# Kernel optimization log

Measured on AMD Instinct MI355X. Metric: run time of the kernel, lower is better.

The kernel has to match this reference:

```python
import jax, jax.numpy as jnp
from jax import lax
import numpy as np

D_MODEL = 1024
N_HEADS = 16
D_STATE = D_MODEL // N_HEADS  # 64
EPS = 1e-6


def setup_inputs() -> dict:
    key = jax.random.key(0)
    ks = jax.random.split(key, 8)
    B, S = 4, 4096
    s = 1.0 / np.sqrt(D_MODEL)
    return {
        "x": jax.random.normal(ks[0], (B, S, D_MODEL), dtype=jnp.float32),
        "state": jnp.zeros((B, N_HEADS, D_STATE), dtype=jnp.float32),
        "norm_w": jnp.ones((D_MODEL,), dtype=jnp.float32),
        "Wp": jax.random.normal(ks[1], (D_MODEL, 3 * N_HEADS * D_STATE), dtype=jnp.float32) * s,
        "bp": jax.random.normal(ks[2], (3 * N_HEADS * D_STATE,), dtype=jnp.float32) * 0.01,
        "Wg": jax.random.normal(ks[3], (D_MODEL, D_MODEL), dtype=jnp.float32) * s,
        "bg": jax.random.normal(ks[4], (D_MODEL,), dtype=jnp.float32) * 0.01,
        "Wo": jax.random.normal(ks[5], (D_MODEL, D_MODEL), dtype=jnp.float32) * s,
        "bo": jax.random.normal(ks[6], (D_MODEL,), dtype=jnp.float32) * 0.01,
    }


def reference(x, state, norm_w, Wp, bp, Wg, bg, Wo, bo):
    B, S, D = x.shape
    # RMSNorm
    rms = jnp.sqrt(jnp.mean(x * x, axis=-1, keepdims=True) + EPS)
    xn = norm_w * x / rms
    # input-dependent gate and SSM parameters (all per-timestep, vectorized)
    gate = jax.nn.sigmoid(xn @ Wg + bg)                        # (B,S,D)
    p = (xn @ Wp + bp).reshape(B, S, N_HEADS, 3, D_STATE)
    delta = jax.nn.sigmoid(p[..., 0, :])                       # (B,S,H,Ds)
    Bt = p[..., 1, :]
    Ct = p[..., 2, :]
    # sequential recurrence h_{t+1} = delta_t * h_t + B_t via lax.scan over time
    def step(h, db):
        d, b = db
        h = d * h + b
        return h, h
    dT = jnp.moveaxis(delta, 1, 0)  # (S,B,H,Ds)
    bT = jnp.moveaxis(Bt, 1, 0)
    new_state, hs = lax.scan(step, state, (dT, bT))
    hs = jnp.moveaxis(hs, 0, 1)     # (B,S,H,Ds)
    ssm = (Ct * hs).reshape(B, S, D)
    mixed = gate * ssm + (1.0 - gate) * xn
    y = mixed @ Wo + bo + x         # out_proj + residual (dropout=0)
    return y, new_state
```

## Files before the change

### kernel.cpp

```cpp
#include <hip/hip_runtime.h>
#include <hip/hip_bf16.h>
#include <cstdint>
#include <cstddef>

#define D_MODEL 1024
#define N_HEADS 16
#define D_STATE 64
#define SEQ 4096
#define BATCH 4
#define M_TOK (BATCH * SEQ)
#define N1 4096
#define CLEN 64
#define NCH (SEQ / CLEN)
#define NCHAN (BATCH * D_MODEL)

typedef __attribute__((ext_vector_type(8))) short bf16x8;
typedef __attribute__((ext_vector_type(4))) short bf16x4;
typedef __attribute__((ext_vector_type(4))) float f32x4;

__device__ __forceinline__ float sigmoidf_(float x) {
    return 1.0f / (1.0f + __expf(-x));
}
__device__ __forceinline__ float b2f(short s) {
    union { float f; unsigned u; } v; v.u = ((unsigned)(unsigned short)s) << 16;
    return v.f;
}
__device__ __forceinline__ short f2b(float f) {
    __hip_bfloat16 h = __float2bfloat16(f);
    return *(short*)&h;
}

__device__ __forceinline__ void async_load16(const void* g, void* l) {
    __builtin_amdgcn_global_load_lds(
        (__attribute__((address_space(1))) void*)(g),
        (__attribute__((address_space(3))) void*)(l), 16, 0, 0);
}

__global__ __launch_bounds__(256) void prep_kernel(
    const float* __restrict__ Wg, const float* __restrict__ Wp,
    const float* __restrict__ Wo,
    const float* __restrict__ x, const float* __restrict__ norm_w,
    __hip_bfloat16* __restrict__ W1T, __hip_bfloat16* __restrict__ WoT,
    __hip_bfloat16* __restrict__ xn)
{
    __shared__ float tile[32][33];
    __shared__ float red[4];
    const int bid = blockIdx.x;
    const int tid = threadIdx.x;

    if (bid < 5120) {
        const float* src; __hip_bfloat16* dst; int N, bx, by, perm;
        if (bid < 1024)      { src = Wg; dst = W1T; N = 1024; bx = bid & 31;          by = bid >> 5;          perm = 0; }
        else if (bid < 4096) { int l = bid - 1024; src = Wp; dst = W1T; N = 3072; bx = l % 96; by = l / 96;   perm = 1; }
        else                 { int l = bid - 4096; src = Wo; dst = WoT; N = 1024; bx = l & 31; by = l >> 5;   perm = 0; }
        int n0 = bx * 32, k0 = by * 32;
        int tx = tid & 31, ty = tid >> 5;
#pragma unroll
        for (int j = 0; j < 32; j += 8)
            tile[ty + j][tx] = src[(size_t)(k0 + ty + j) * N + n0 + tx];
        __syncthreads();
#pragma unroll
        for (int j = 0; j < 32; j += 8) {
            int n = n0 + ty + j;
            int row;
            if (perm) {
                int ht = n >> 6;
                row = 1024 + (ht % 3) * 1024 + (ht / 3) * 64 + (n & 63);
            } else row = n;
            dst[(size_t)row * D_MODEL + k0 + tx] = __float2bfloat16(tile[tx][ty + j]);
        }
    } else {
        int m = bid - 5120;
        const float4* xr = (const float4*)(x + (size_t)m * D_MODEL);
        float4 v = xr[tid];
        float ss = v.x * v.x + v.y * v.y + v.z * v.z + v.w * v.w;
#pragma unroll
        for (int o = 32; o >= 1; o >>= 1) ss += __shfl_xor(ss, o, 64);
        int wave = tid >> 6, lane = tid & 63;
        if (lane == 0) red[wave] = ss;
        __syncthreads();
        float tot = red[0] + red[1] + red[2] + red[3];
        float scale = rsqrtf(tot * (1.0f / D_MODEL) + 1e-6f);
        const float4* wr = (const float4*)norm_w;
        float4 wv = wr[tid];
        __hip_bfloat16 o4[4];
        o4[0] = __float2bfloat16(wv.x * v.x * scale);
        o4[1] = __float2bfloat16(wv.y * v.y * scale);
        o4[2] = __float2bfloat16(wv.z * v.z * scale);
        o4[3] = __float2bfloat16(wv.w * v.w * scale);
        *(uint64_t*)(xn + (size_t)m * D_MODEL + tid * 4) = *(uint64_t*)o4;
    }
}

template <int MODE>
__global__ __launch_bounds__(512, 2) void gemm256(
    const __hip_bfloat16* __restrict__ A,
    const __hip_bfloat16* __restrict__ Bt,
    const float* __restrict__ bias0,
    const float* __restrict__ bias1,
    void* __restrict__ outp, int N, int K)
{
    extern __shared__ short lds[];
    const int tid = threadIdx.x;
    const int wave = tid >> 6, lane = tid & 63;
    const int fr = lane & 15, fq = lane >> 4;
    const int frx = fr & 7;
    const int wm = (wave >> 2) * 128;
    const int wn = (wave & 3) * 64;

    const int gx = gridDim.x;
    const int nwg = gx * gridDim.y;
    const int orig = blockIdx.y * gx + blockIdx.x;
    const int swz = (orig & 7) * (nwg >> 3) + (orig >> 3);
    const int m0 = (swz / gx) * 256;
    const int n0 = (swz % gx) * 256;

    const int rb = tid >> 3, p8 = tid & 7;
    const int lsl = p8 ^ (rb & 7);
    const short* Ag0 = (const short*)A + (size_t)(m0 + rb) * K + lsl * 8;
    const short* Bg0 = (const short*)Bt + (size_t)(n0 + rb) * K + lsl * 8;
    const int stL = rb * 64 + p8 * 8;

    const int laneA = (wm + fr) * 128;
    const int laneB = (wn + fr) * 128;
    const int F0 = (fq ^ frx) * 16;
    const int F1 = ((4 + fq) ^ frx) * 16;

    const int NT = K >> 6;

    f32x4 acc[2][4][4];
#pragma unroll
    for (int h = 0; h < 2; ++h)
#pragma unroll
        for (int i = 0; i < 4; ++i)
#pragma unroll
            for (int j = 0; j < 4; ++j)
                acc[h][i][j] = (f32x4){0.f, 0.f, 0.f, 0.f};

    {
        short* la = lds;
        short* lb = lds + 16384;
        async_load16(Bg0 + (size_t)(0 * 64) * K, lb + stL + 0 * 4096);
        async_load16(Bg0 + (size_t)(1 * 64) * K, lb + stL + 1 * 4096);
        async_load16(Bg0 + (size_t)(2 * 64) * K, lb + stL + 2 * 4096);
        async_load16(Bg0 + (size_t)(3 * 64) * K, lb + stL + 3 * 4096);
        async_load16(Ag0 + (size_t)(0 * 64) * K, la + stL + 0 * 4096);
        async_load16(Ag0 + (size_t)(2 * 64) * K, la + stL + 2 * 4096);
        async_load16(Ag0 + (size_t)(1 * 64) * K, la + stL + 1 * 4096);
        async_load16(Ag0 + (size_t)(3 * 64) * K, la + stL + 3 * 4096);
    }
    asm volatile("s_waitcnt vmcnt(2)" ::: "memory");
    __builtin_amdgcn_s_barrier();
    __builtin_amdgcn_sched_barrier(0);

#define RD(base, off) (*(const bf16x8*)((base) + (off)))
#define STAGE_A(c) async_load16(AgN + (size_t)((c) * 64) * K, laN + stL + (c) * 4096)
#define STAGE_B(c) async_load16(BgN + (size_t)((c) * 64) * K, lbN + stL + (c) * 4096)

    bf16x8 afA[4][2], afB[4][2], b0[2][2], b1[2][2];

    {
        const char* bA0 = (const char*)lds + laneA + F0;
        const char* bA1 = (const char*)lds + laneA + F1;
        const char* bB0 = (const char*)(lds + 16384) + laneB + F0;
        const char* bB1 = (const char*)(lds + 16384) + laneB + F1;
#pragma unroll
        for (int i = 0; i < 4; ++i) { afA[i][0] = RD(bA0, i * 2048); afA[i][1] = RD(bA1, i * 2048); }
#pragma unroll
        for (int j = 0; j < 2; ++j) { b0[j][0] = RD(bB0, j * 2048); b0[j][1] = RD(bB1, j * 2048); }
    }

    for (int t = 0; t < NT; ++t) {
        const short* Ab = lds + ((t & 1) ? 32768 : 0);
        const short* Bb = Ab + 16384;
        short* laN = lds + ((t & 1) ? 0 : 32768);
        short* lbN = laN + 16384;
        const short* AgN = Ag0 + (size_t)(t + 1) * 64;
        const short* BgN = Bg0 + (size_t)(t + 1) * 64;
        const bool pf = (t + 1 < NT);
        const char* bA0 = (const char*)Ab + laneA + F0;
        const char* bA1 = (const char*)Ab + laneA + F1;
        const char* bB0 = (const char*)Bb + laneB + F0;
        const char* bB1 = (const char*)Bb + laneB + F1;

        if (pf) { STAGE_B(0); STAGE_B(1); }
#pragma unroll
        for (int j = 0; j < 2; ++j) { b1[j][0] = RD(bB0, (2 + j) * 2048); b1[j][1] = RD(bB1, (2 + j) * 2048); }
        __builtin_amdgcn_s_setprio(1);
#pragma unroll
        for (int i = 0; i < 4; ++i)
#pragma unroll
            for (int j = 0; j < 2; ++j) {
                acc[0][i][j] = __builtin_amdgcn_mfma_f32_16x16x32_bf16(afA[i][0], b0[j][0], acc[0][i][j], 0, 0, 0);
                acc[0][i][j] = __builtin_amdgcn_mfma_f32_16x16x32_bf16(afA[i][1], b0[j][1], acc[0][i][j], 0, 0, 0);
            }
        __builtin_amdgcn_s_setprio(0);
        __builtin_amdgcn_sched_barrier(0);

        if (pf) { STAGE_B(2); STAGE_B(3); }
        if (pf) { asm volatile("s_waitcnt vmcnt(4)" ::: "memory"); }
        else    { asm volatile("s_waitcnt vmcnt(0)" ::: "memory"); }
        __builtin_amdgcn_s_barrier();
        __builtin_amdgcn_sched_barrier(0);
#pragma unroll
        for (int i = 0; i < 4; ++i) { afB[i][0] = RD(bA0, 8192 + i * 2048); afB[i][1] = RD(bA1, 8192 + i * 2048); }
        __builtin_amdgcn_s_setprio(1);
#pragma unroll
        for (int i = 0; i < 4; ++i)
#pragma unroll
            for (int j = 0; j < 2; ++j) {
                acc[0][i][2 + j] = __builtin_amdgcn_mfma_f32_16x16x32_bf16(afA[i][0], b1[j][0], acc[0][i][2 + j], 0, 0, 0);
                acc[0][i][2 + j] = __builtin_amdgcn_mfma_f32_16x16x32_bf16(afA[i][1], b1[j][1], acc[0][i][2 + j], 0, 0, 0);
            }
        __builtin_amdgcn_s_setprio(0);
        __builtin_amdgcn_sched_barrier(0);

        if (pf) { STAGE_A(0); STAGE_A(2); }
        __builtin_amdgcn_s_setprio(1);
#pragma unroll
        for (int i = 0; i < 4; ++i)
#pragma unroll
            for (int j = 0; j < 2; ++j) {
                acc[1][i][j] = __builtin_amdgcn_mfma_f32_16x16x32_bf16(afB[i][0], b0[j][0], acc[1][i][j], 0, 0, 0);
                acc[1][i][j] = __builtin_amdgcn_mfma_f32_16x16x32_bf16(afB[i][1], b0[j][1], acc[1][i][j], 0, 0, 0);
            }
        __builtin_amdgcn_s_setprio(0);
        __builtin_amdgcn_sched_barrier(0);

        if (pf) {
            STAGE_A(1); STAGE_A(3);
            asm volatile("s_waitcnt vmcnt(2)" ::: "memory");
            __builtin_amdgcn_s_barrier();
            __builtin_amdgcn_sched_barrier(0);
            const char* nA0 = (const char*)laN + laneA + F0;
            const char* nA1 = (const char*)laN + laneA + F1;
            const char* nB0 = (const char*)lbN + laneB + F0;
            const char* nB1 = (const char*)lbN + laneB + F1;
#pragma unroll
            for (int i = 0; i < 4; ++i) { afA[i][0] = RD(nA0, i * 2048); afA[i][1] = RD(nA1, i * 2048); }
#pragma unroll
            for (int j = 0; j < 2; ++j) { b0[j][0] = RD(nB0, j * 2048); b0[j][1] = RD(nB1, j * 2048); }
        }
        __builtin_amdgcn_s_setprio(1);
#pragma unroll
        for (int i = 0; i < 4; ++i)
#pragma unroll
            for (int j = 0; j < 2; ++j) {
                acc[1][i][2 + j] = __builtin_amdgcn_mfma_f32_16x16x32_bf16(afB[i][0], b1[j][0], acc[1][i][2 + j], 0, 0, 0);
                acc[1][i][2 + j] = __builtin_amdgcn_mfma_f32_16x16x32_bf16(afB[i][1], b1[j][1], acc[1][i][2 + j], 0, 0, 0);
            }
        __builtin_amdgcn_s_setprio(0);
        __builtin_amdgcn_sched_barrier(0);
    }
#undef RD
#undef STAGE_A
#undef STAGE_B

    if constexpr (MODE == 0) {
        __hip_bfloat16* O = (__hip_bfloat16*)outp;
        float bv[4];
#pragma unroll
        for (int j = 0; j < 4; ++j) {
            int gcol = n0 + wn + j * 16 + fr;
            if (gcol < D_MODEL) bv[j] = bias0[gcol];
            else {
                int q = gcol - D_MODEL;
                int tt = q >> 10, hd = q & 1023;
                bv[j] = bias1[(hd >> 6) * 192 + tt * 64 + (hd & 63)];
            }
        }
#pragma unroll
        for (int h = 0; h < 2; ++h)
#pragma unroll
            for (int i = 0; i < 4; ++i)
#pragma unroll
                for (int r = 0; r < 4; ++r) {
                    int grow = m0 + wm + h * 64 + i * 16 + fq * 4 + r;
                    __hip_bfloat16* orow = O + (size_t)grow * N + n0 + wn + fr;
#pragma unroll
                    for (int j = 0; j < 4; ++j)
                        orow[j * 16] = __float2bfloat16(acc[h][i][j][r] + bv[j]);
                }
    } else {
        float* O = (float*)outp;
#pragma unroll
        for (int h = 0; h < 2; ++h)
#pragma unroll
            for (int i = 0; i < 4; ++i)
#pragma unroll
                for (int r = 0; r < 4; ++r) {
                    int grow = m0 + wm + h * 64 + i * 16 + fq * 4 + r;
#pragma unroll
                    for (int j = 0; j < 4; ++j) {
                        int gcol = n0 + wn + j * 16 + fr;
                        O[(size_t)grow * N + gcol] =
                            acc[h][i][j][r] + bias0[gcol] + bias1[(size_t)grow * D_MODEL + gcol];
                    }
                }
    }
}

__global__ __launch_bounds__(256) void scan_part1(
    const __hip_bfloat16* __restrict__ out1,
    float* __restrict__ Abuf, float* __restrict__ Bbuf)
{
    int g = blockIdx.x * 256 + threadIdx.x;
    int cg = g & 1023;
    int c = g >> 10;
    int chan0 = cg * 4;
    int b = chan0 >> 10, hd0 = chan0 & 1023;
    size_t tok0 = (size_t)b * SEQ + (size_t)c * CLEN;
    const short* pd = (const short*)out1 + tok0 * N1 + D_MODEL + hd0;
    float a[4] = {1.f, 1.f, 1.f, 1.f};
    float hl[4] = {0.f, 0.f, 0.f, 0.f};
#pragma unroll 4
    for (int s = 0; s < CLEN; s++) {
        bf16x4 dv = *(const bf16x4*)pd;
        bf16x4 bv = *(const bf16x4*)(pd + 1024);
#pragma unroll
        for (int k = 0; k < 4; k++) {
            float sd = sigmoidf_(b2f(dv[k]));
            a[k] *= sd;
            hl[k] = sd * hl[k] + b2f(bv[k]);
        }
        pd += N1;
    }
    *(f32x4*)&Abuf[c * NCHAN + chan0] = (f32x4){a[0], a[1], a[2], a[3]};
    *(f32x4*)&Bbuf[c * NCHAN + chan0] = (f32x4){hl[0], hl[1], hl[2], hl[3]};
}

__global__ __launch_bounds__(256) void scan_apply(
    const __hip_bfloat16* __restrict__ out1,
    const __hip_bfloat16* __restrict__ xn,
    const float* __restrict__ Abuf, const float* __restrict__ Bbuf,
    const float* __restrict__ state,
    __hip_bfloat16* __restrict__ mixed, float* __restrict__ new_state)
{
    int g = blockIdx.x * 256 + threadIdx.x;
    int cg = g & 1023;
    int c = g >> 10;
    int chan0 = cg * 4;
    int b = chan0 >> 10, hd0 = chan0 & 1023;
    size_t tok0 = (size_t)b * SEQ + (size_t)c * CLEN;

    f32x4 hp4 = *(const f32x4*)&state[chan0];
    for (int cc = 0; cc < c; ++cc) {
        f32x4 av = *(const f32x4*)&Abuf[cc * NCHAN + chan0];
        f32x4 bv = *(const f32x4*)&Bbuf[cc * NCHAN + chan0];
        hp4 = av * hp4 + bv;
    }
    float hp[4] = {hp4[0], hp4[1], hp4[2], hp4[3]};

    const short* rbase = (const short*)out1 + tok0 * N1;
    const short* xb = (const short*)xn + tok0 * D_MODEL + hd0;
    short* mb = (short*)mixed + tok0 * D_MODEL + hd0;
#pragma unroll 4
    for (int s = 0; s < CLEN; s++) {
        bf16x4 dv = *(const bf16x4*)(rbase + D_MODEL + hd0);
        bf16x4 bv = *(const bf16x4*)(rbase + 2048 + hd0);
        bf16x4 cv = *(const bf16x4*)(rbase + 3072 + hd0);
        bf16x4 gv = *(const bf16x4*)(rbase + hd0);
        bf16x4 xv = *(const bf16x4*)xb;
        bf16x4 ov;
#pragma unroll
        for (int k = 0; k < 4; k++) {
            float sd = sigmoidf_(b2f(dv[k]));
            hp[k] = sd * hp[k] + b2f(bv[k]);
            float gg = sigmoidf_(b2f(gv[k]));
            ov[k] = f2b(gg * (b2f(cv[k]) * hp[k]) + (1.0f - gg) * b2f(xv[k]));
        }
        *(bf16x4*)mb = ov;
        rbase += N1;
        xb += D_MODEL;
        mb += D_MODEL;
    }
    if (c == NCH - 1)
        *(f32x4*)&new_state[chan0] = (f32x4){hp[0], hp[1], hp[2], hp[3]};
}

extern "C" void kernel_launch(void* const* d_in, const int* in_sizes, int n_in,
                              void* d_out, int out_size, void* d_ws, size_t ws_size,
                              hipStream_t stream) {
    const float* x      = (const float*)d_in[0];
    const float* state  = (const float*)d_in[1];
    const float* norm_w = (const float*)d_in[2];
    const float* Wp     = (const float*)d_in[3];
    const float* bp     = (const float*)d_in[4];
    const float* Wg     = (const float*)d_in[5];
    const float* bg     = (const float*)d_in[6];
    const float* Wo     = (const float*)d_in[7];
    const float* bo     = (const float*)d_in[8];
    float* out = (float*)d_out;

    __hip_bfloat16* W1T   = (__hip_bfloat16*)d_ws;
    __hip_bfloat16* WoT   = W1T + (size_t)N1 * D_MODEL;
    __hip_bfloat16* xnb   = WoT + (size_t)D_MODEL * D_MODEL;
    __hip_bfloat16* out1  = xnb + (size_t)M_TOK * D_MODEL;
    __hip_bfloat16* mixed = out1 + (size_t)M_TOK * N1;
    float* Abuf = (float*)(mixed + (size_t)M_TOK * D_MODEL);
    float* Bbuf = Abuf + (size_t)NCHAN * NCH;

    static bool attr_set = false;
    if (!attr_set) {
        hipFuncSetAttribute(reinterpret_cast<const void*>(&gemm256<0>),
                            hipFuncAttributeMaxDynamicSharedMemorySize, 131072);
        hipFuncSetAttribute(reinterpret_cast<const void*>(&gemm256<1>),
                            hipFuncAttributeMaxDynamicSharedMemorySize, 131072);
        attr_set = true;
    }

    prep_kernel<<<5120 + M_TOK, 256, 0, stream>>>(
        Wg, Wp, Wo, x, norm_w, W1T, WoT, xnb);

    gemm256<0><<<dim3(N1 / 256, M_TOK / 256), 512, 131072, stream>>>(
        xnb, W1T, bg, bp, (void*)out1, N1, D_MODEL);

    scan_part1<<<(NCHAN / 4 * NCH) / 256, 256, 0, stream>>>(out1, Abuf, Bbuf);

    scan_apply<<<(NCHAN / 4 * NCH) / 256, 256, 0, stream>>>(
        out1, xnb, Abuf, Bbuf, state, mixed, out + (size_t)M_TOK * D_MODEL);

    gemm256<1><<<dim3(D_MODEL / 256, M_TOK / 256), 512, 131072, stream>>>(
        mixed, WoT, bo, x, (void*)out, D_MODEL, D_MODEL);
}
```

Baseline: 392.7 us.

## Restage GEMM loads two tiles ahead, shrink scan chunks, write mixed in place

The GEMM prefetch is restructured so whole 64-wide K tiles are loaded two iterations ahead into the alternate LDS buffer, with a single barrier per iteration instead of interleaved partial stages. The scan chunk length is halved to expose more parallelism in the chunked recurrence, and the mixed output now overwrites the normalized-input buffer in place, dropping a separate workspace. The RMSNorm part of the prep kernel now processes one row per wave, removing the shared-memory reduction and block sync. The deeper prefetch trades finer-grained overlap for fewer barriers, and shorter chunks add more serial carry work per chunk in the apply pass.

```diff
diff --git a/kernel.cpp b/kernel.cpp
--- a/kernel.cpp
+++ b/kernel.cpp
@@ -10,7 +10,7 @@
 #define BATCH 4
 #define M_TOK (BATCH * SEQ)
 #define N1 4096
-#define CLEN 64
+#define CLEN 32
 #define NCH (SEQ / CLEN)
 #define NCHAN (BATCH * D_MODEL)
 
@@ -44,15 +44,14 @@
     __hip_bfloat16* __restrict__ xn)
 {
     __shared__ float tile[32][33];
-    __shared__ float red[4];
     const int bid = blockIdx.x;
     const int tid = threadIdx.x;
 
     if (bid < 5120) {
         const float* src; __hip_bfloat16* dst; int N, bx, by, perm;
-        if (bid < 1024)      { src = Wg; dst = W1T; N = 1024; bx = bid & 31;          by = bid >> 5;          perm = 0; }
-        else if (bid < 4096) { int l = bid - 1024; src = Wp; dst = W1T; N = 3072; bx = l % 96; by = l / 96;   perm = 1; }
-        else                 { int l = bid - 4096; src = Wo; dst = WoT; N = 1024; bx = l & 31; by = l >> 5;   perm = 0; }
+        if (bid < 1024)      { src = Wg; dst = W1T; N = 1024; bx = bid & 31;        by = bid >> 5;        perm = 0; }
+        else if (bid < 4096) { int l = bid - 1024; src = Wp; dst = W1T; N = 3072; bx = l % 96; by = l / 96; perm = 1; }
+        else                 { int l = bid - 4096; src = Wo; dst = WoT; N = 1024; bx = l & 31; by = l >> 5; perm = 0; }
         int n0 = bx * 32, k0 = by * 32;
         int tx = tid & 31, ty = tid >> 5;
 #pragma unroll
@@ -70,25 +69,30 @@
             dst[(size_t)row * D_MODEL + k0 + tx] = __float2bfloat16(tile[tx][ty + j]);
         }
     } else {
-        int m = bid - 5120;
+        int m = (bid - 5120) * 4 + (tid >> 6);
+        int lane = tid & 63;
         const float4* xr = (const float4*)(x + (size_t)m * D_MODEL);
-        float4 v = xr[tid];
-        float ss = v.x * v.x + v.y * v.y + v.z * v.z + v.w * v.w;
+        float4 v[4];
+        float ss = 0.f;
+#pragma unroll
+        for (int q = 0; q < 4; ++q) {
+            v[q] = xr[lane + 64 * q];
+            ss += v[q].x * v[q].x + v[q].y * v[q].y + v[q].z * v[q].z + v[q].w * v[q].w;
+        }
 #pragma unroll
         for (int o = 32; o >= 1; o >>= 1) ss += __shfl_xor(ss, o, 64);
-        int wave = tid >> 6, lane = tid & 63;
-        if (lane == 0) red[wave] = ss;
-        __syncthreads();
-        float tot = red[0] + red[1] + red[2] + red[3];
-        float scale = rsqrtf(tot * (1.0f / D_MODEL) + 1e-6f);
+        float scale = rsqrtf(ss * (1.0f / D_MODEL) + 1e-6f);
         const float4* wr = (const float4*)norm_w;
-        float4 wv = wr[tid];
-        __hip_bfloat16 o4[4];
-        o4[0] = __float2bfloat16(wv.x * v.x * scale);
-        o4[1] = __float2bfloat16(wv.y * v.y * scale);
-        o4[2] = __float2bfloat16(wv.z * v.z * scale);
-        o4[3] = __float2bfloat16(wv.w * v.w * scale);
-        *(uint64_t*)(xn + (size_t)m * D_MODEL + tid * 4) = *(uint64_t*)o4;
+#pragma unroll
+        for (int q = 0; q < 4; ++q) {
+            float4 wv = wr[lane + 64 * q];
+            __hip_bfloat16 o4[4];
+            o4[0] = __float2bfloat16(wv.x * v[q].x * scale);
+            o4[1] = __float2bfloat16(wv.y * v[q].y * scale);
+            o4[2] = __float2bfloat16(wv.z * v[q].z * scale);
+            o4[3] = __float2bfloat16(wv.w * v[q].w * scale);
+            *(uint64_t*)(xn + (size_t)m * D_MODEL + (lane + 64 * q) * 4) = *(uint64_t*)o4;
+        }
     }
 }
 
@@ -137,28 +141,30 @@
             for (int j = 0; j < 4; ++j)
                 acc[h][i][j] = (f32x4){0.f, 0.f, 0.f, 0.f};
 
-    {
-        short* la = lds;
-        short* lb = lds + 16384;
-        async_load16(Bg0 + (size_t)(0 * 64) * K, lb + stL + 0 * 4096);
-        async_load16(Bg0 + (size_t)(1 * 64) * K, lb + stL + 1 * 4096);
-        async_load16(Bg0 + (size_t)(2 * 64) * K, lb + stL + 2 * 4096);
-        async_load16(Bg0 + (size_t)(3 * 64) * K, lb + stL + 3 * 4096);
-        async_load16(Ag0 + (size_t)(0 * 64) * K, la + stL + 0 * 4096);
-        async_load16(Ag0 + (size_t)(2 * 64) * K, la + stL + 2 * 4096);
-        async_load16(Ag0 + (size_t)(1 * 64) * K, la + stL + 1 * 4096);
-        async_load16(Ag0 + (size_t)(3 * 64) * K, la + stL + 3 * 4096);
-    }
-    asm volatile("s_waitcnt vmcnt(2)" ::: "memory");
+#define STAGE8(Tt, base)                                                   \
+    {                                                                      \
+        short* la_ = (base);                                               \
+        short* lb_ = (base) + 16384;                                       \
+        const short* Ag_ = Ag0 + (size_t)(Tt) * 64;                        \
+        const short* Bg_ = Bg0 + (size_t)(Tt) * 64;                        \
+        async_load16(Bg_ + (size_t)(0 * 64) * K, lb_ + stL + 0 * 4096);    \
+        async_load16(Bg_ + (size_t)(1 * 64) * K, lb_ + stL + 1 * 4096);    \
+        async_load16(Bg_ + (size_t)(2 * 64) * K, lb_ + stL + 2 * 4096);    \
+        async_load16(Bg_ + (size_t)(3 * 64) * K, lb_ + stL + 3 * 4096);    \
+        async_load16(Ag_ + (size_t)(0 * 64) * K, la_ + stL + 0 * 4096);    \
+        async_load16(Ag_ + (size_t)(1 * 64) * K, la_ + stL + 1 * 4096);    \
+        async_load16(Ag_ + (size_t)(2 * 64) * K, la_ + stL + 2 * 4096);    \
+        async_load16(Ag_ + (size_t)(3 * 64) * K, la_ + stL + 3 * 4096);    \
+    }
+#define RD(base, off) (*(const bf16x8*)((base) + (off)))
+
+    STAGE8(0, lds);
+    STAGE8(1, lds + 32768);
+    asm volatile("s_waitcnt vmcnt(8)" ::: "memory");
     __builtin_amdgcn_s_barrier();
     __builtin_amdgcn_sched_barrier(0);
 
-#define RD(base, off) (*(const bf16x8*)((base) + (off)))
-#define STAGE_A(c) async_load16(AgN + (size_t)((c) * 64) * K, laN + stL + (c) * 4096)
-#define STAGE_B(c) async_load16(BgN + (size_t)((c) * 64) * K, lbN + stL + (c) * 4096)
-
     bf16x8 afA[4][2], afB[4][2], b0[2][2], b1[2][2];
-
     {
         const char* bA0 = (const char*)lds + laneA + F0;
         const char* bA1 = (const char*)lds + laneA + F1;
@@ -171,19 +177,16 @@
     }
 
     for (int t = 0; t < NT; ++t) {
-        const short* Ab = lds + ((t & 1) ? 32768 : 0);
+        const int par = t & 1;
+        const short* Ab = lds + (par ? 32768 : 0);
         const short* Bb = Ab + 16384;
-        short* laN = lds + ((t & 1) ? 0 : 32768);
-        short* lbN = laN + 16384;
-        const short* AgN = Ag0 + (size_t)(t + 1) * 64;
-        const short* BgN = Bg0 + (size_t)(t + 1) * 64;
-        const bool pf = (t + 1 < NT);
         const char* bA0 = (const char*)Ab + laneA + F0;
         const char* bA1 = (const char*)Ab + laneA + F1;
         const char* bB0 = (const char*)Bb + laneB + F0;
         const char* bB1 = (const char*)Bb + laneB + F1;
-
-        if (pf) { STAGE_B(0); STAGE_B(1); }
+        const bool pf = (t + 1 < NT);
+        const bool pf2 = (t + 2 < NT);
+
 #pragma unroll
         for (int j = 0; j < 2; ++j) { b1[j][0] = RD(bB0, (2 + j) * 2048); b1[j][1] = RD(bB1, (2 + j) * 2048); }
         __builtin_amdgcn_s_setprio(1);
@@ -197,11 +200,6 @@
         __builtin_amdgcn_s_setprio(0);
         __builtin_amdgcn_sched_barrier(0);
 
-        if (pf) { STAGE_B(2); STAGE_B(3); }
-        if (pf) { asm volatile("s_waitcnt vmcnt(4)" ::: "memory"); }
-        else    { asm volatile("s_waitcnt vmcnt(0)" ::: "memory"); }
-        __builtin_amdgcn_s_barrier();
-        __builtin_amdgcn_sched_barrier(0);
 #pragma unroll
         for (int i = 0; i < 4; ++i) { afB[i][0] = RD(bA0, 8192 + i * 2048); afB[i][1] = RD(bA1, 8192 + i * 2048); }
         __builtin_amdgcn_s_setprio(1);
@@ -215,7 +213,6 @@
         __builtin_amdgcn_s_setprio(0);
         __builtin_amdgcn_sched_barrier(0);
 
-        if (pf) { STAGE_A(0); STAGE_A(2); }
         __builtin_amdgcn_s_setprio(1);
 #pragma unroll
         for (int i = 0; i < 4; ++i)
@@ -228,18 +225,20 @@
         __builtin_amdgcn_sched_barrier(0);
 
         if (pf) {
-            STAGE_A(1); STAGE_A(3);
-            asm volatile("s_waitcnt vmcnt(2)" ::: "memory");
+            asm volatile("s_waitcnt vmcnt(0)" ::: "memory");
             __builtin_amdgcn_s_barrier();
             __builtin_amdgcn_sched_barrier(0);
-            const char* nA0 = (const char*)laN + laneA + F0;
-            const char* nA1 = (const char*)laN + laneA + F1;
-            const char* nB0 = (const char*)lbN + laneB + F0;
-            const char* nB1 = (const char*)lbN + laneB + F1;
+            if (pf2) STAGE8(t + 2, lds + (par ? 32768 : 0));
+            const char* nA0 = (const char*)(lds + (par ? 0 : 32768)) + laneA + F0;
+            const char* nA1 = (const char*)(lds + (par ? 0 : 32768)) + laneA + F1;
+            const char* nB0 = (const char*)(lds + (par ? 16384 : 49152)) + laneB + F0;
+            const char* nB1 = (const char*)(lds + (par ? 16384 : 49152)) + laneB + F1;
 #pragma unroll
             for (int i = 0; i < 4; ++i) { afA[i][0] = RD(nA0, i * 2048); afA[i][1] = RD(nA1, i * 2048); }
 #pragma unroll
             for (int j = 0; j < 2; ++j) { b0[j][0] = RD(nB0, j * 2048); b0[j][1] = RD(nB1, j * 2048); }
+        } else {
+            asm volatile("s_waitcnt vmcnt(0)" ::: "memory");
         }
         __builtin_amdgcn_s_setprio(1);
 #pragma unroll
@@ -253,8 +252,7 @@
         __builtin_amdgcn_sched_barrier(0);
     }
 #undef RD
-#undef STAGE_A
-#undef STAGE_B
+#undef STAGE8
 
     if constexpr (MODE == 0) {
         __hip_bfloat16* O = (__hip_bfloat16*)outp;
@@ -331,10 +329,10 @@
 
 __global__ __launch_bounds__(256) void scan_apply(
     const __hip_bfloat16* __restrict__ out1,
-    const __hip_bfloat16* __restrict__ xn,
+    __hip_bfloat16* xnm,
     const float* __restrict__ Abuf, const float* __restrict__ Bbuf,
     const float* __restrict__ state,
-    __hip_bfloat16* __restrict__ mixed, float* __restrict__ new_state)
+    float* __restrict__ new_state)
 {
     int g = blockIdx.x * 256 + threadIdx.x;
     int cg = g & 1023;
@@ -352,8 +350,7 @@
     float hp[4] = {hp4[0], hp4[1], hp4[2], hp4[3]};
 
     const short* rbase = (const short*)out1 + tok0 * N1;
-    const short* xb = (const short*)xn + tok0 * D_MODEL + hd0;
-    short* mb = (short*)mixed + tok0 * D_MODEL + hd0;
+    short* xb = (short*)xnm + tok0 * D_MODEL + hd0;
 #pragma unroll 4
     for (int s = 0; s < CLEN; s++) {
         bf16x4 dv = *(const bf16x4*)(rbase + D_MODEL + hd0);
@@ -369,10 +366,9 @@
             float gg = sigmoidf_(b2f(gv[k]));
             ov[k] = f2b(gg * (b2f(cv[k]) * hp[k]) + (1.0f - gg) * b2f(xv[k]));
         }
-        *(bf16x4*)mb = ov;
+        *(bf16x4*)xb = ov;
         rbase += N1;
         xb += D_MODEL;
-        mb += D_MODEL;
     }
     if (c == NCH - 1)
         *(f32x4*)&new_state[chan0] = (f32x4){hp[0], hp[1], hp[2], hp[3]};
@@ -396,8 +392,7 @@
     __hip_bfloat16* WoT   = W1T + (size_t)N1 * D_MODEL;
     __hip_bfloat16* xnb   = WoT + (size_t)D_MODEL * D_MODEL;
     __hip_bfloat16* out1  = xnb + (size_t)M_TOK * D_MODEL;
-    __hip_bfloat16* mixed = out1 + (size_t)M_TOK * N1;
-    float* Abuf = (float*)(mixed + (size_t)M_TOK * D_MODEL);
+    float* Abuf = (float*)(out1 + (size_t)M_TOK * N1);
     float* Bbuf = Abuf + (size_t)NCHAN * NCH;
 
     static bool attr_set = false;
@@ -409,7 +404,7 @@
         attr_set = true;
     }
 
-    prep_kernel<<<5120 + M_TOK, 256, 0, stream>>>(
+    prep_kernel<<<9216, 256, 0, stream>>>(
         Wg, Wp, Wo, x, norm_w, W1T, WoT, xnb);
 
     gemm256<0><<<dim3(N1 / 256, M_TOK / 256), 512, 131072, stream>>>(
@@ -418,8 +413,8 @@
     scan_part1<<<(NCHAN / 4 * NCH) / 256, 256, 0, stream>>>(out1, Abuf, Bbuf);
 
     scan_apply<<<(NCHAN / 4 * NCH) / 256, 256, 0, stream>>>(
-        out1, xnb, Abuf, Bbuf, state, mixed, out + (size_t)M_TOK * D_MODEL);
+        out1, xnb, Abuf, Bbuf, state, out + (size_t)M_TOK * D_MODEL);
 
     gemm256<1><<<dim3(D_MODEL / 256, M_TOK / 256), 512, 131072, stream>>>(
-        mixed, WoT, bo, x, (void*)out, D_MODEL, D_MODEL);
-}
+        xnb, WoT, bo, x, (void*)out, D_MODEL, D_MODEL);
+}
```

After: 400.7 us. 1.02x slower.

## Halve scan chunk length, wave-per-row RMSNorm, in-place mixed output, split first GEMM

Applied to the files above, without the earlier changes.

Halves the scan chunk length so the chunked scan has more parallel chunks and shorter serial loops, at the cost of a longer carry-prefix loop in scan_apply. RMSNorm now uses one wave per token instead of a 256-thread block, which removes the shared-memory reduction and the barrier. scan_apply writes the mixed activations in place over the normalized input buffer, dropping a separate workspace buffer. The first GEMM is split into four launches over token slices, which adds launch overhead and gives no clear reuse benefit.

```diff
diff --git a/kernel.cpp b/kernel.cpp
--- a/kernel.cpp
+++ b/kernel.cpp
@@ -10,7 +10,7 @@
 #define BATCH 4
 #define M_TOK (BATCH * SEQ)
 #define N1 4096
-#define CLEN 64
+#define CLEN 32
 #define NCH (SEQ / CLEN)
 #define NCHAN (BATCH * D_MODEL)
 
@@ -44,15 +44,14 @@
     __hip_bfloat16* __restrict__ xn)
 {
     __shared__ float tile[32][33];
-    __shared__ float red[4];
     const int bid = blockIdx.x;
     const int tid = threadIdx.x;
 
     if (bid < 5120) {
         const float* src; __hip_bfloat16* dst; int N, bx, by, perm;
-        if (bid < 1024)      { src = Wg; dst = W1T; N = 1024; bx = bid & 31;          by = bid >> 5;          perm = 0; }
-        else if (bid < 4096) { int l = bid - 1024; src = Wp; dst = W1T; N = 3072; bx = l % 96; by = l / 96;   perm = 1; }
-        else                 { int l = bid - 4096; src = Wo; dst = WoT; N = 1024; bx = l & 31; by = l >> 5;   perm = 0; }
+        if (bid < 1024)      { src = Wg; dst = W1T; N = 1024; bx = bid & 31;        by = bid >> 5;        perm = 0; }
+        else if (bid < 4096) { int l = bid - 1024; src = Wp; dst = W1T; N = 3072; bx = l % 96; by = l / 96; perm = 1; }
+        else                 { int l = bid - 4096; src = Wo; dst = WoT; N = 1024; bx = l & 31; by = l >> 5; perm = 0; }
         int n0 = bx * 32, k0 = by * 32;
         int tx = tid & 31, ty = tid >> 5;
 #pragma unroll
@@ -70,25 +69,30 @@
             dst[(size_t)row * D_MODEL + k0 + tx] = __float2bfloat16(tile[tx][ty + j]);
         }
     } else {
-        int m = bid - 5120;
+        int m = (bid - 5120) * 4 + (tid >> 6);
+        int lane = tid & 63;
         const float4* xr = (const float4*)(x + (size_t)m * D_MODEL);
-        float4 v = xr[tid];
-        float ss = v.x * v.x + v.y * v.y + v.z * v.z + v.w * v.w;
+        float4 v[4];
+        float ss = 0.f;
+#pragma unroll
+        for (int q = 0; q < 4; ++q) {
+            v[q] = xr[lane + 64 * q];
+            ss += v[q].x * v[q].x + v[q].y * v[q].y + v[q].z * v[q].z + v[q].w * v[q].w;
+        }
 #pragma unroll
         for (int o = 32; o >= 1; o >>= 1) ss += __shfl_xor(ss, o, 64);
-        int wave = tid >> 6, lane = tid & 63;
-        if (lane == 0) red[wave] = ss;
-        __syncthreads();
-        float tot = red[0] + red[1] + red[2] + red[3];
-        float scale = rsqrtf(tot * (1.0f / D_MODEL) + 1e-6f);
+        float scale = rsqrtf(ss * (1.0f / D_MODEL) + 1e-6f);
         const float4* wr = (const float4*)norm_w;
-        float4 wv = wr[tid];
-        __hip_bfloat16 o4[4];
-        o4[0] = __float2bfloat16(wv.x * v.x * scale);
-        o4[1] = __float2bfloat16(wv.y * v.y * scale);
-        o4[2] = __float2bfloat16(wv.z * v.z * scale);
-        o4[3] = __float2bfloat16(wv.w * v.w * scale);
-        *(uint64_t*)(xn + (size_t)m * D_MODEL + tid * 4) = *(uint64_t*)o4;
+#pragma unroll
+        for (int q = 0; q < 4; ++q) {
+            float4 wv = wr[lane + 64 * q];
+            __hip_bfloat16 o4[4];
+            o4[0] = __float2bfloat16(wv.x * v[q].x * scale);
+            o4[1] = __float2bfloat16(wv.y * v[q].y * scale);
+            o4[2] = __float2bfloat16(wv.z * v[q].z * scale);
+            o4[3] = __float2bfloat16(wv.w * v[q].w * scale);
+            *(uint64_t*)(xn + (size_t)m * D_MODEL + (lane + 64 * q) * 4) = *(uint64_t*)o4;
+        }
     }
 }
 
@@ -98,7 +102,7 @@
     const __hip_bfloat16* __restrict__ Bt,
     const float* __restrict__ bias0,
     const float* __restrict__ bias1,
-    void* __restrict__ outp, int N, int K)
+    void* __restrict__ outp, int N, int K, int moff)
 {
     extern __shared__ short lds[];
     const int tid = threadIdx.x;
@@ -112,7 +116,7 @@
     const int nwg = gx * gridDim.y;
     const int orig = blockIdx.y * gx + blockIdx.x;
     const int swz = (orig & 7) * (nwg >> 3) + (orig >> 3);
-    const int m0 = (swz / gx) * 256;
+    const int m0 = (swz / gx) * 256 + moff;
     const int n0 = (swz % gx) * 256;
 
     const int rb = tid >> 3, p8 = tid & 7;
@@ -331,10 +335,10 @@
 
 __global__ __launch_bounds__(256) void scan_apply(
     const __hip_bfloat16* __restrict__ out1,
-    const __hip_bfloat16* __restrict__ xn,
+    __hip_bfloat16* xnm,
     const float* __restrict__ Abuf, const float* __restrict__ Bbuf,
     const float* __restrict__ state,
-    __hip_bfloat16* __restrict__ mixed, float* __restrict__ new_state)
+    float* __restrict__ new_state)
 {
     int g = blockIdx.x * 256 + threadIdx.x;
     int cg = g & 1023;
@@ -352,8 +356,7 @@
     float hp[4] = {hp4[0], hp4[1], hp4[2], hp4[3]};
 
     const short* rbase = (const short*)out1 + tok0 * N1;
-    const short* xb = (const short*)xn + tok0 * D_MODEL + hd0;
-    short* mb = (short*)mixed + tok0 * D_MODEL + hd0;
+    short* xb = (short*)xnm + tok0 * D_MODEL + hd0;
 #pragma unroll 4
     for (int s = 0; s < CLEN; s++) {
         bf16x4 dv = *(const bf16x4*)(rbase + D_MODEL + hd0);
@@ -369,10 +372,9 @@
             float gg = sigmoidf_(b2f(gv[k]));
             ov[k] = f2b(gg * (b2f(cv[k]) * hp[k]) + (1.0f - gg) * b2f(xv[k]));
         }
-        *(bf16x4*)mb = ov;
+        *(bf16x4*)xb = ov;
         rbase += N1;
         xb += D_MODEL;
-        mb += D_MODEL;
     }
     if (c == NCH - 1)
         *(f32x4*)&new_state[chan0] = (f32x4){hp[0], hp[1], hp[2], hp[3]};
@@ -396,8 +398,7 @@
     __hip_bfloat16* WoT   = W1T + (size_t)N1 * D_MODEL;
     __hip_bfloat16* xnb   = WoT + (size_t)D_MODEL * D_MODEL;
     __hip_bfloat16* out1  = xnb + (size_t)M_TOK * D_MODEL;
-    __hip_bfloat16* mixed = out1 + (size_t)M_TOK * N1;
-    float* Abuf = (float*)(mixed + (size_t)M_TOK * D_MODEL);
+    float* Abuf = (float*)(out1 + (size_t)M_TOK * N1);
     float* Bbuf = Abuf + (size_t)NCHAN * NCH;
 
     static bool attr_set = false;
@@ -409,17 +410,18 @@
         attr_set = true;
     }
 
-    prep_kernel<<<5120 + M_TOK, 256, 0, stream>>>(
+    prep_kernel<<<9216, 256, 0, stream>>>(
         Wg, Wp, Wo, x, norm_w, W1T, WoT, xnb);
 
-    gemm256<0><<<dim3(N1 / 256, M_TOK / 256), 512, 131072, stream>>>(
-        xnb, W1T, bg, bp, (void*)out1, N1, D_MODEL);
+    for (int s = 0; s < 4; ++s)
+        gemm256<0><<<dim3(N1 / 256, 16), 512, 131072, stream>>>(
+            xnb, W1T, bg, bp, (void*)out1, N1, D_MODEL, s * 4096);
 
     scan_part1<<<(NCHAN / 4 * NCH) / 256, 256, 0, stream>>>(out1, Abuf, Bbuf);
 
     scan_apply<<<(NCHAN / 4 * NCH) / 256, 256, 0, stream>>>(
-        out1, xnb, Abuf, Bbuf, state, mixed, out + (size_t)M_TOK * D_MODEL);
+        out1, xnb, Abuf, Bbuf, state, out + (size_t)M_TOK * D_MODEL);
 
     gemm256<1><<<dim3(D_MODEL / 256, M_TOK / 256), 512, 131072, stream>>>(
-        mixed, WoT, bo, x, (void*)out, D_MODEL, D_MODEL);
-}
+        xnb, WoT, bo, x, (void*)out, D_MODEL, D_MODEL, 0);
+}
```

Result: no change. 398.5 us (+1.5%).
